# Optimization experiments

Measured on AMD Instinct MI355X. Metric: run time of the kernel, lower is better.

## Reference

```python
import jax, jax.numpy as jnp
import numpy as np

B, S, E = 4, 2048, 1024
H, D = 16, 64  # num_heads, attention_head_dim


def setup_inputs() -> dict:
    key = jax.random.key(0)
    ks = jax.random.split(key, 9)
    scale_e = 1.0 / np.sqrt(E)
    scale_hd = 1.0 / np.sqrt(H * D)
    x = jax.random.normal(ks[0], (B, S, E), dtype=jnp.float32)
    # per-head projection weights, stacked: [H, E, D]
    Wq = jax.random.uniform(ks[1], (H, E, D), minval=-scale_e, maxval=scale_e, dtype=jnp.float32)
    Wk = jax.random.uniform(ks[2], (H, E, D), minval=-scale_e, maxval=scale_e, dtype=jnp.float32)
    Wv = jax.random.uniform(ks[3], (H, E, D), minval=-scale_e, maxval=scale_e, dtype=jnp.float32)
    bq = jax.random.uniform(ks[4], (H, D), minval=-scale_e, maxval=scale_e, dtype=jnp.float32)
    bk = jax.random.uniform(ks[5], (H, D), minval=-scale_e, maxval=scale_e, dtype=jnp.float32)
    bv = jax.random.uniform(ks[6], (H, D), minval=-scale_e, maxval=scale_e, dtype=jnp.float32)
    Wo = jax.random.uniform(ks[7], (H * D, E), minval=-scale_hd, maxval=scale_hd, dtype=jnp.float32)
    bo = jax.random.uniform(ks[8], (E,), minval=-scale_hd, maxval=scale_hd, dtype=jnp.float32)
    return {"x": x, "Wq": Wq, "Wk": Wk, "Wv": Wv, "bq": bq, "bk": bk, "bv": bv, "Wo": Wo, "bo": bo}


def reference(x, Wq, Wk, Wv, bq, bk, bv, Wo, bo):
    # Per-head QKV projections, vectorized over heads: [B,H,S,D]
    Q = jnp.einsum('bse,hed->bhsd', x, Wq) + bq[None, :, None, :]
    K = jnp.einsum('bse,hed->bhsd', x, Wk) + bk[None, :, None, :]
    V = jnp.einsum('bse,hed->bhsd', x, Wv) + bv[None, :, None, :]
    scale = 1.0 / jnp.sqrt(jnp.asarray(D, dtype=Q.dtype))
    scores = jnp.einsum('bhsd,bhtd->bhst', Q, K) * scale  # [B,H,S,S]
    attn = jax.nn.softmax(scores, axis=-1)
    Z = jnp.einsum('bhst,bhtd->bhsd', attn, V)            # [B,H,S,D]
    # concat heads on feature dim -> [B,S,H*D], then output projection
    Zc = jnp.transpose(Z, (0, 2, 1, 3)).reshape(B, S, H * D)
    return Zc @ Wo + bo
```

## Files before the change

kernel.cpp:

```cpp
#include <hip/hip_runtime.h>


typedef __attribute__((ext_vector_type(4)))  float   f32x4;
typedef __attribute__((ext_vector_type(16))) float   f32x16;
typedef __attribute__((ext_vector_type(8)))  __bf16  bf16x8;
typedef __attribute__((ext_vector_type(4)))  __bf16  bf16x4;
typedef __attribute__((ext_vector_type(4)))  unsigned int u32x4;
typedef unsigned int u32;

#if __has_builtin(__builtin_amdgcn_exp2f)
#define EXP2F(x) __builtin_amdgcn_exp2f(x)
#else
#define EXP2F(x) exp2f(x)
#endif

__device__ __forceinline__ f32x4 fzero4() {
    f32x4 z = {0.f, 0.f, 0.f, 0.f};
    return z;
}
__device__ __forceinline__ f32x16 fzero16() {
    f32x16 z;
#pragma unroll
    for (int i = 0; i < 16; i++) z[i] = 0.f;
    return z;
}

__device__ __forceinline__ u32 cvtpk_bf16(float lo, float hi_) {
    u32 r;
    asm("v_cvt_pk_bf16_f32 %0, %1, %2" : "=v"(r) : "v"(lo), "v"(hi_));
    return r;
}

__device__ __forceinline__ void gload_lds16(const void* g, void* l) {
    __builtin_amdgcn_global_load_lds(
        (const __attribute__((address_space(1))) u32*)g,
        (__attribute__((address_space(3))) u32*)l, 16, 0, 0);
}

__global__ __launch_bounds__(256) void cvt_f32_bf16_4(
    const float* __restrict__ s, __bf16* __restrict__ d, long n) {
    long i = ((long)blockIdx.x * 256 + threadIdx.x) * 4;
    if (i >= n) return;
    float4 v = *(const float4*)(s + i);
    bf16x4 o = { (__bf16)v.x, (__bf16)v.y, (__bf16)v.z, (__bf16)v.w };
    *(bf16x4*)(d + i) = o;
}

__global__ __launch_bounds__(256) void pack_w_t(
    const float* __restrict__ src, __bf16* __restrict__ dst, int R, int C) {
    __shared__ float t[32][33];
    const int z = blockIdx.z;
    src += (size_t)z * R * C;
    dst += (size_t)z * R * C;
    const int r0 = blockIdx.x * 32, c0 = blockIdx.y * 32;
    const int x = threadIdx.x, y = threadIdx.y;
#pragma unroll
    for (int i = 0; i < 4; i++)
        t[y + i * 8][x] = src[(size_t)(r0 + y + i * 8) * C + c0 + x];
    __syncthreads();
#pragma unroll
    for (int i = 0; i < 4; i++)
        dst[(size_t)(c0 + y + i * 8) * R + r0 + x] = (__bf16)t[x][y + i * 8];
}

__global__ __launch_bounds__(256) void pack_bias(
    const float* __restrict__ bq, const float* __restrict__ bk,
    const float* __restrict__ bv, float* __restrict__ bqkv) {
    int n = blockIdx.x * 256 + threadIdx.x;
    if (n >= 3072) return;
    int t = n >> 10, r = n & 1023;
    const float* s = (t == 0) ? bq : (t == 1) ? bk : bv;
    bqkv[n] = s[r];
}

#define GEMM_STAGE(BUF, KOFF)                                                  \
  {                                                                            \
    gload_lds16(A + arow0 * K + (KOFF) + kcol,                                 \
                (char*)As + (BUF) * 16384 + wid * 1024);                       \
    gload_lds16(A + arow1 * K + (KOFF) + kcol,                                 \
                (char*)As + (BUF) * 16384 + 8192 + wid * 1024);                \
    gload_lds16(Bt + brow * K + (KOFF) + kcol,                                 \
                (char*)Bs + (BUF) * 8192 + wid * 1024);                        \
  }

#define GEMM_COMPUTE(BUF)                                                      \
  {                                                                            \
    bf16x8 a[4], b[4];                                                         \
    _Pragma("unroll")                                                          \
    for (int mi = 0; mi < 4; mi++)                                             \
      a[mi] = *(const bf16x8*)&As[(BUF) * 8192 +                               \
                                  (mr * 64 + mi * 16 + l15) * 32 + l4 * 8];    \
    _Pragma("unroll")                                                          \
    for (int ni = 0; ni < 4; ni++)                                             \
      b[ni] = *(const bf16x8*)&Bs[(BUF) * 4096 +                               \
                                  (nc * 64 + ni * 16 + l15) * 32 + l4 * 8];    \
    _Pragma("unroll")                                                          \
    for (int mi = 0; mi < 4; mi++)                                             \
      _Pragma("unroll")                                                        \
      for (int ni = 0; ni < 4; ni++)                                           \
        acc[mi][ni] = __builtin_amdgcn_mfma_f32_16x16x32_bf16(                 \
            a[mi], b[ni], acc[mi][ni], 0, 0, 0);                               \
  }

#define GEMM_PREAMBLE                                                          \
    const int tid  = threadIdx.x;                                              \
    const int lane = tid & 63, wid = tid >> 6;                                 \
    const int mr = wid >> 1, nc = wid & 1;                                     \
    const int l15 = lane & 15, l4 = lane >> 4;                                 \
    const int bn = blockIdx.x, bm = blockIdx.y;                                \
    const long arow0 = (long)bm * 256 + (tid >> 2);                            \
    const long arow1 = arow0 + 128;                                            \
    const long brow  = (long)bn * 128 + (tid >> 2);                            \
    const int  kcol  = (tid & 3) * 8;                                          \
    f32x4 acc[4][4];                                                           \
    _Pragma("unroll")                                                          \
    for (int i = 0; i < 4; i++)                                                \
      _Pragma("unroll")                                                        \
      for (int j = 0; j < 4; j++) acc[i][j] = fzero4();                        \
    GEMM_STAGE(0, 0)                                                           \
    __syncthreads();                                                           \
    int cur = 0;                                                               \
    for (int k0 = 0; k0 < K; k0 += 32, cur ^= 1) {                             \
        if (k0 + 32 < K) GEMM_STAGE(cur ^ 1, k0 + 32)                          \
        GEMM_COMPUTE(cur)                                                      \
        __syncthreads();                                                       \
    }

template <bool F32OUT>
__global__ __launch_bounds__(512) void gemm_bt(
    const __bf16* __restrict__ A, const __bf16* __restrict__ Bt,
    const float* __restrict__ bias, void* __restrict__ Cout,
    int M, int N, int K, int ldc) {
    __shared__ __bf16 As[2 * 256 * 32];
    __shared__ __bf16 Bs[2 * 128 * 32];
    GEMM_PREAMBLE

#pragma unroll
    for (int mi = 0; mi < 4; mi++)
#pragma unroll
        for (int ni = 0; ni < 4; ni++) {
            const int row = bm * 256 + mr * 64 + mi * 16 + l4 * 4;
            const int col = bn * 128 + nc * 64 + ni * 16 + l15;
            const float bv = bias ? bias[col] : 0.f;
#pragma unroll
            for (int r = 0; r < 4; r++) {
                float v = acc[mi][ni][r] + bv;
                if (F32OUT)
                    ((float*)Cout)[(long)(row + r) * ldc + col] = v;
                else
                    ((__bf16*)Cout)[(long)(row + r) * ldc + col] = (__bf16)v;
            }
        }
}

__global__ __launch_bounds__(512) void gemm_qkv(
    const __bf16* __restrict__ A, const __bf16* __restrict__ Bt,
    const float* __restrict__ bias, __bf16* __restrict__ QKV,
    __bf16* __restrict__ VT, int K) {
    __shared__ __bf16 As[2 * 256 * 32];
    __shared__ __bf16 Bs[2 * 128 * 32];
    GEMM_PREAMBLE

    if (bn < 16) {
#pragma unroll
        for (int mi = 0; mi < 4; mi++)
#pragma unroll
            for (int ni = 0; ni < 4; ni++) {
                const int row = bm * 256 + mr * 64 + mi * 16 + l4 * 4;
                const int col = bn * 128 + nc * 64 + ni * 16 + l15;
                const float bv = bias[col];
#pragma unroll
                for (int r = 0; r < 4; r++)
                    QKV[(long)(row + r) * 3072 + col] =
                        (__bf16)(acc[mi][ni][r] + bv);
            }
    } else {
#pragma unroll
        for (int mi = 0; mi < 4; mi++)
#pragma unroll
            for (int ni = 0; ni < 4; ni++) {
                const int row = bm * 256 + mr * 64 + mi * 16 + l4 * 4;
                const int col = bn * 128 + nc * 64 + ni * 16 + l15;
                const float bv = bias[col];
                const int vcol = col - 2048;
                const int h = vcol >> 6, dcol = vcol & 63;
                const int bb = row >> 11, s = row & 2047;
                bf16x4 o;
#pragma unroll
                for (int r = 0; r < 4; r++)
                    o[r] = (__bf16)(acc[mi][ni][r] + bv);
                *(bf16x4*)&VT[((size_t)(bb * 16 + h) * 64 + dcol) * 2048 + s] = o;
            }
    }
}

#define ATTN_SM_PV(S0, S1, M_R, L_R, O0, O1)                                   \
  {                                                                            \
    float mm[16];                                                              \
    _Pragma("unroll")                                                          \
    for (int i = 0; i < 16; i++) mm[i] = fmaxf(S0[i], S1[i]);                  \
    _Pragma("unroll")                                                          \
    for (int st = 8; st >= 1; st >>= 1)                                        \
      _Pragma("unroll")                                                        \
      for (int i = 0; i < st; i++) mm[i] = fmaxf(mm[i], mm[i + st]);           \
    const float pm = fmaxf(mm[0], __shfl_xor(mm[0], 32));                      \
    if (!__all(pm - M_R <= 64.f)) {              \
      const float mnew = fmaxf(M_R, pm);                                       \
      const float alpha = EXP2F((M_R - mnew) * csc);                           \
      M_R = mnew;                                                              \
      L_R *= alpha;                                                            \
      _Pragma("unroll")                                                        \
      for (int i = 0; i < 16; i++) { O0[i] *= alpha; O1[i] *= alpha; }         \
    }                                                                          \
    const float mc = M_R * csc;                                                \
    float ss[16];                                                              \
    _Pragma("unroll")                                                          \
    for (int i = 0; i < 16; i++) {                                             \
      float p0 = EXP2F(S0[i] * csc - mc); S0[i] = p0;                          \
      float p1 = EXP2F(S1[i] * csc - mc); S1[i] = p1;                          \
      ss[i] = p0 + p1;                                                         \
    }                                                                          \
    _Pragma("unroll")                                                          \
    for (int st = 8; st >= 1; st >>= 1)                                        \
      _Pragma("unroll")                                                        \
      for (int i = 0; i < st; i++) ss[i] += ss[i + st];                        \
    L_R += ss[0] + __shfl_xor(ss[0], 32);                                      \
    __builtin_amdgcn_s_setprio(1);                                             \
    _Pragma("unroll")                                                          \
    for (int kkt = 0; kkt < 4; kkt++) {                                        \
      const int r0 = (kkt & 1) * 8;                                            \
      u32 w0, w1, w2, w3;                                                      \
      if (kkt < 2) {                                                           \
        w0 = cvtpk_bf16(S0[r0],     S0[r0 + 1]);                               \
        w1 = cvtpk_bf16(S0[r0 + 2], S0[r0 + 3]);                               \
        w2 = cvtpk_bf16(S0[r0 + 4], S0[r0 + 5]);                               \
        w3 = cvtpk_bf16(S0[r0 + 6], S0[r0 + 7]);                               \
      } else {                                                                 \
        w0 = cvtpk_bf16(S1[r0],     S1[r0 + 1]);                               \
        w1 = cvtpk_bf16(S1[r0 + 2], S1[r0 + 3]);                               \
        w2 = cvtpk_bf16(S1[r0 + 4], S1[r0 + 5]);                               \
        w3 = cvtpk_bf16(S1[r0 + 6], S1[r0 + 7]);                               \
      }                                                                        \
      asm("v_permlane32_swap_b32 %0, %1" : "+v"(w0), "+v"(w2));                \
      asm("v_permlane32_swap_b32 %0, %1" : "+v"(w1), "+v"(w3));                \
      u32x4 pw = {w0, w1, w2, w3};                                             \
      bf16x8 pf = __builtin_bit_cast(bf16x8, pw);                              \
      O0 = __builtin_amdgcn_mfma_f32_32x32x16_bf16(vf[kkt],     pf, O0, 0, 0, 0); \
      O1 = __builtin_amdgcn_mfma_f32_32x32x16_bf16(vf[4 + kkt], pf, O1, 0, 0, 0); \
    }                                                                          \
    __builtin_amdgcn_s_setprio(0);                                             \
  }

#define ATTN_EPI(O0, O1, L_R, ROWBASE)                                         \
  {                                                                            \
    const float inv = 1.0f / L_R;                                              \
    _Pragma("unroll")                                                          \
    for (int g = 0; g < 4; g++) {                                              \
      bf16x4 t4a, t4b;                                                         \
      _Pragma("unroll")                                                        \
      for (int j = 0; j < 4; j++) {                                            \
        t4a[j] = (__bf16)(O0[4 * g + j] * inv);                                \
        t4b[j] = (__bf16)(O1[4 * g + j] * inv);                                \
      }                                                                        \
      *(bf16x4*)&Tl[trow][g * 8 + hi * 4]      = t4a;                          \
      *(bf16x4*)&Tl[trow][32 + g * 8 + hi * 4] = t4b;                          \
    }                                                                          \
    asm volatile("s_waitcnt lgkmcnt(0)" ::: "memory");                         \
    __builtin_amdgcn_sched_barrier(0);                                         \
    _Pragma("unroll")                                                          \
    for (int i = 0; i < 4; i++) {                                              \
      bf16x8 z = *(const bf16x8*)&Tl[rr][ch + i * 8];                          \
      *(bf16x8*)&Z[((size_t)b * S + (ROWBASE) + rr) * 1024 + h * 64 +          \
                   ch + i * 8] = z;                                            \
    }                                                                          \
    asm volatile("s_waitcnt lgkmcnt(0)" ::: "memory");                         \
    __builtin_amdgcn_sched_barrier(0);                                         \
  }

__global__ __launch_bounds__(256, 2) void attn_fwd(
    const __bf16* __restrict__ QKV, const __bf16* __restrict__ VT,
    __bf16* __restrict__ Z) {
    const int S = 2048, LDQ = 3072;
    const int dd = blockIdx.x;
    const int blk = (dd & 7) * 64 + (dd >> 3);
    const int qt = blk & 7, bh = blk >> 3, b = bh >> 4, h = bh & 15;
    const int tid = threadIdx.x, wid = tid >> 6, lane = tid & 63;
    const int l31 = lane & 31, hi = lane >> 5;

    __shared__ __bf16 smem[16384];

    const __bf16* Qb = QKV + (size_t)b * S * LDQ + h * 64;
    const __bf16* Kb = Qb + 1024;
    const __bf16* Vb = VT + (size_t)bh * 64 * S;
    const int qrowA = qt * 256 + wid * 32;
    const int qrowB = qrowA + 128;

    bf16x8 qfA[4], qfB[4];
#pragma unroll
    for (int kk = 0; kk < 4; kk++) {
        qfA[kk] = *(const bf16x8*)(Qb + (size_t)(qrowA + l31) * LDQ + kk * 16 + hi * 8);
        qfB[kk] = *(const bf16x8*)(Qb + (size_t)(qrowB + l31) * LDQ + kk * 16 + hi * 8);
    }

    const int f0 = wid * 2, f1 = wid * 2 + 1;
    const int kr0 = (f0 >> 2) * 32 + l31, kc0 = (f0 & 3) * 16 + hi * 8;
    const int kr1 = (f1 >> 2) * 32 + l31, kc1 = (f1 & 3) * 16 + hi * 8;
    const int vr0 = kr0, vs0 = kc0;
    const int vr1 = kr1, vs1 = kc1;
    const int ldst = lane * 16;

    f32x16 oA0 = fzero16(), oA1 = fzero16();
    f32x16 oB0 = fzero16(), oB1 = fzero16();
    float m_rA = -1e30f, l_rA = 0.f, m_rB = -1e30f, l_rB = 0.f;
    const float csc = 0.18033688011f;

    gload_lds16(Kb + (size_t)kr0 * LDQ + kc0, (char*)smem + f0 * 1024 + ldst);
    gload_lds16(Kb + (size_t)kr1 * LDQ + kc1, (char*)smem + f1 * 1024 + ldst);
    gload_lds16(Vb + (size_t)vr0 * S + vs0,   (char*)smem + 16384 + f0 * 1024 + ldst);
    gload_lds16(Vb + (size_t)vr1 * S + vs1,   (char*)smem + 16384 + f1 * 1024 + ldst);
    asm volatile("s_waitcnt vmcnt(0)" ::: "memory");
    __syncthreads();

    int cur = 0;
    for (int t0 = 0; t0 < S; t0 += 64, cur ^= 1) {
        if (t0 + 64 < S) {
            char* kl = (char*)smem + (cur ^ 1) * 8192;
            char* vl = (char*)smem + 16384 + (cur ^ 1) * 8192;
            gload_lds16(Kb + (size_t)(t0 + 64 + kr0) * LDQ + kc0, kl + f0 * 1024 + ldst);
            gload_lds16(Kb + (size_t)(t0 + 64 + kr1) * LDQ + kc1, kl + f1 * 1024 + ldst);
            gload_lds16(Vb + (size_t)vr0 * S + t0 + 64 + vs0,     vl + f0 * 1024 + ldst);
            gload_lds16(Vb + (size_t)vr1 * S + t0 + 64 + vs1,     vl + f1 * 1024 + ldst);
        }
        const char* kbase = (const char*)smem + cur * 8192;
        const char* vbase = (const char*)smem + 16384 + cur * 8192;

        bf16x8 kf[8];
#pragma unroll
        for (int f = 0; f < 8; f++)
            kf[f] = *(const bf16x8*)(kbase + f * 1024 + ldst);
        f32x16 sA0 = fzero16(), sA1 = fzero16();
        f32x16 sB0 = fzero16(), sB1 = fzero16();
        __builtin_amdgcn_s_setprio(1);
#pragma unroll
        for (int kk = 0; kk < 4; kk++) {
            sA0 = __builtin_amdgcn_mfma_f32_32x32x16_bf16(kf[kk],     qfA[kk], sA0, 0, 0, 0);
            sA1 = __builtin_amdgcn_mfma_f32_32x32x16_bf16(kf[4 + kk], qfA[kk], sA1, 0, 0, 0);
        }
#pragma unroll
        for (int kk = 0; kk < 4; kk++) {
            sB0 = __builtin_amdgcn_mfma_f32_32x32x16_bf16(kf[kk],     qfB[kk], sB0, 0, 0, 0);
            sB1 = __builtin_amdgcn_mfma_f32_32x32x16_bf16(kf[4 + kk], qfB[kk], sB1, 0, 0, 0);
        }
        __builtin_amdgcn_s_setprio(0);

        bf16x8 vf[8];
#pragma unroll
        for (int f = 0; f < 8; f++)
            vf[f] = *(const bf16x8*)(vbase + f * 1024 + ldst);

        ATTN_SM_PV(sA0, sA1, m_rA, l_rA, oA0, oA1)
        ATTN_SM_PV(sB0, sB1, m_rB, l_rB, oB0, oB1)

        asm volatile("s_waitcnt vmcnt(0)" ::: "memory");
        __syncthreads();
    }

    __bf16 (*Tl)[72] = (__bf16 (*)[72])smem;
    const int trow = wid * 32 + l31;
    const int rr = wid * 32 + (lane >> 1);
    const int ch = (lane & 1) * 32;
    ATTN_EPI(oA0, oA1, l_rA, qt * 256)
    ATTN_EPI(oB0, oB1, l_rB, qt * 256 + 128)
}

extern "C" void kernel_launch(void* const* d_in, const int* in_sizes, int n_in,
                              void* d_out, int out_size, void* d_ws, size_t ws_size,
                              hipStream_t stream) {
    const float* x  = (const float*)d_in[0];
    const float* Wq = (const float*)d_in[1];
    const float* Wk = (const float*)d_in[2];
    const float* Wv = (const float*)d_in[3];
    const float* bq = (const float*)d_in[4];
    const float* bk = (const float*)d_in[5];
    const float* bv = (const float*)d_in[6];
    const float* Wo = (const float*)d_in[7];
    const float* bo = (const float*)d_in[8];
    float* out = (float*)d_out;

    char* p = (char*)d_ws;
    __bf16* xb   = (__bf16*)p; p += 8192L * 1024 * 2;
    __bf16* Wqkv = (__bf16*)p; p += 3072L * 1024 * 2;
    float*  bqkv = (float*)p;  p += 3072L * 4;
    __bf16* QKV  = (__bf16*)p; p += 8192L * 3072 * 2;
    __bf16* VTb  = (__bf16*)p; p += 64L * 64 * 2048 * 2;
    __bf16* Zb   = (__bf16*)p; p += 8192L * 1024 * 2;
    __bf16* Wot  = (__bf16*)p; p += 1024L * 1024 * 2;

    cvt_f32_bf16_4<<<8192, 256, 0, stream>>>(x, xb, 8192L * 1024);
    pack_w_t<<<dim3(32, 2, 16), dim3(32, 8), 0, stream>>>(Wq, Wqkv,                1024, 64);
    pack_w_t<<<dim3(32, 2, 16), dim3(32, 8), 0, stream>>>(Wk, Wqkv + 1024L * 1024, 1024, 64);
    pack_w_t<<<dim3(32, 2, 16), dim3(32, 8), 0, stream>>>(Wv, Wqkv + 2048L * 1024, 1024, 64);
    pack_w_t<<<dim3(32, 32, 1), dim3(32, 8), 0, stream>>>(Wo, Wot, 1024, 1024);
    pack_bias<<<12, 256, 0, stream>>>(bq, bk, bv, bqkv);

    gemm_qkv<<<dim3(24, 32), 512, 0, stream>>>(xb, Wqkv, bqkv, QKV, VTb, 1024);
    attn_fwd<<<512, 256, 0, stream>>>(QKV, VTb, Zb);
    gemm_bt<true><<<dim3(8, 32), 512, 0, stream>>>(Zb, Wot, bo, out,
                                                   8192, 1024, 1024, 1024);
}
```

Baseline: 220.1 us.

## Fuse x fp32-to-bf16 conversion into QKV GEMM and remap block tiles per XCD

```diff
diff --git a/kernel.cpp b/kernel.cpp
--- a/kernel.cpp
+++ b/kernel.cpp
@@ -35,15 +35,6 @@
     __builtin_amdgcn_global_load_lds(
         (const __attribute__((address_space(1))) u32*)g,
         (__attribute__((address_space(3))) u32*)l, 16, 0, 0);
-}
-
-__global__ __launch_bounds__(256) void cvt_f32_bf16_4(
-    const float* __restrict__ s, __bf16* __restrict__ d, long n) {
-    long i = ((long)blockIdx.x * 256 + threadIdx.x) * 4;
-    if (i >= n) return;
-    float4 v = *(const float4*)(s + i);
-    bf16x4 o = { (__bf16)v.x, (__bf16)v.y, (__bf16)v.z, (__bf16)v.w };
-    *(bf16x4*)(d + i) = o;
 }
 
 __global__ __launch_bounds__(256) void pack_w_t(
@@ -72,6 +63,25 @@
     const float* s = (t == 0) ? bq : (t == 1) ? bk : bv;
     bqkv[n] = s[r];
 }
+
+#define GEMM_COMPUTE(BUF)                                                      \
+  {                                                                            \
+    bf16x8 a[4], b[4];                                                         \
+    _Pragma("unroll")                                                          \
+    for (int mi = 0; mi < 4; mi++)                                             \
+      a[mi] = *(const bf16x8*)&As[(BUF) * 8192 +                               \
+                                  (mr * 64 + mi * 16 + l15) * 32 + l4 * 8];    \
+    _Pragma("unroll")                                                          \
+    for (int ni = 0; ni < 4; ni++)                                             \
+      b[ni] = *(const bf16x8*)&Bs[(BUF) * 4096 +                               \
+                                  (nc * 64 + ni * 16 + l15) * 32 + l4 * 8];    \
+    _Pragma("unroll")                                                          \
+    for (int mi = 0; mi < 4; mi++)                                             \
+      _Pragma("unroll")                                                        \
+      for (int ni = 0; ni < 4; ni++)                                           \
+        acc[mi][ni] = __builtin_amdgcn_mfma_f32_16x16x32_bf16(                 \
+            a[mi], b[ni], acc[mi][ni], 0, 0, 0);                               \
+  }
 
 #define GEMM_STAGE(BUF, KOFF)                                                  \
   {                                                                            \
@@ -83,49 +93,6 @@
                 (char*)Bs + (BUF) * 8192 + wid * 1024);                        \
   }
 
-#define GEMM_COMPUTE(BUF)                                                      \
-  {                                                                            \
-    bf16x8 a[4], b[4];                                                         \
-    _Pragma("unroll")                                                          \
-    for (int mi = 0; mi < 4; mi++)                                             \
-      a[mi] = *(const bf16x8*)&As[(BUF) * 8192 +                               \
-                                  (mr * 64 + mi * 16 + l15) * 32 + l4 * 8];    \
-    _Pragma("unroll")                                                          \
-    for (int ni = 0; ni < 4; ni++)                                             \
-      b[ni] = *(const bf16x8*)&Bs[(BUF) * 4096 +                               \
-                                  (nc * 64 + ni * 16 + l15) * 32 + l4 * 8];    \
-    _Pragma("unroll")                                                          \
-    for (int mi = 0; mi < 4; mi++)                                             \
-      _Pragma("unroll")                                                        \
-      for (int ni = 0; ni < 4; ni++)                                           \
-        acc[mi][ni] = __builtin_amdgcn_mfma_f32_16x16x32_bf16(                 \
-            a[mi], b[ni], acc[mi][ni], 0, 0, 0);                               \
-  }
-
-#define GEMM_PREAMBLE                                                          \
-    const int tid  = threadIdx.x;                                              \
-    const int lane = tid & 63, wid = tid >> 6;                                 \
-    const int mr = wid >> 1, nc = wid & 1;                                     \
-    const int l15 = lane & 15, l4 = lane >> 4;                                 \
-    const int bn = blockIdx.x, bm = blockIdx.y;                                \
-    const long arow0 = (long)bm * 256 + (tid >> 2);                            \
-    const long arow1 = arow0 + 128;                                            \
-    const long brow  = (long)bn * 128 + (tid >> 2);                            \
-    const int  kcol  = (tid & 3) * 8;                                          \
-    f32x4 acc[4][4];                                                           \
-    _Pragma("unroll")                                                          \
-    for (int i = 0; i < 4; i++)                                                \
-      _Pragma("unroll")                                                        \
-      for (int j = 0; j < 4; j++) acc[i][j] = fzero4();                        \
-    GEMM_STAGE(0, 0)                                                           \
-    __syncthreads();                                                           \
-    int cur = 0;                                                               \
-    for (int k0 = 0; k0 < K; k0 += 32, cur ^= 1) {                             \
-        if (k0 + 32 < K) GEMM_STAGE(cur ^ 1, k0 + 32)                          \
-        GEMM_COMPUTE(cur)                                                      \
-        __syncthreads();                                                       \
-    }
-
 template <bool F32OUT>
 __global__ __launch_bounds__(512) void gemm_bt(
     const __bf16* __restrict__ A, const __bf16* __restrict__ Bt,
@@ -133,7 +100,31 @@
     int M, int N, int K, int ldc) {
     __shared__ __bf16 As[2 * 256 * 32];
     __shared__ __bf16 Bs[2 * 128 * 32];
-    GEMM_PREAMBLE
+    const int tid  = threadIdx.x;
+    const int lane = tid & 63, wid = tid >> 6;
+    const int mr = wid >> 1, nc = wid & 1;
+    const int l15 = lane & 15, l4 = lane >> 4;
+    const int dd = blockIdx.x;
+    const int idx = dd >> 3;
+    const int bm = (dd & 7) * 4 + (idx >> 3), bn = idx & 7;
+    const long arow0 = (long)bm * 256 + (tid >> 2);
+    const long arow1 = arow0 + 128;
+    const long brow  = (long)bn * 128 + (tid >> 2);
+    const int  kcol  = (tid & 3) * 8;
+    f32x4 acc[4][4];
+#pragma unroll
+    for (int i = 0; i < 4; i++)
+#pragma unroll
+        for (int j = 0; j < 4; j++) acc[i][j] = fzero4();
+
+    GEMM_STAGE(0, 0)
+    __syncthreads();
+    int cur = 0;
+    for (int k0 = 0; k0 < K; k0 += 32, cur ^= 1) {
+        if (k0 + 32 < K) GEMM_STAGE(cur ^ 1, k0 + 32)
+        GEMM_COMPUTE(cur)
+        __syncthreads();
+    }
 
 #pragma unroll
     for (int mi = 0; mi < 4; mi++)
@@ -153,13 +144,70 @@
         }
 }
 
+#define QKV_A_LOAD(KOFF)                                                       \
+    float4 a00 = *(const float4*)(Xr0 + (KOFF) + kcol);                        \
+    float4 a01 = *(const float4*)(Xr0 + (KOFF) + kcol + 4);                    \
+    float4 a10 = *(const float4*)(Xr1 + (KOFF) + kcol);                        \
+    float4 a11 = *(const float4*)(Xr1 + (KOFF) + kcol + 4);
+
+#define QKV_A_WRITE(BUF)                                                       \
+  {                                                                            \
+    bf16x8 w0 = {(__bf16)a00.x, (__bf16)a00.y, (__bf16)a00.z, (__bf16)a00.w,   \
+                 (__bf16)a01.x, (__bf16)a01.y, (__bf16)a01.z, (__bf16)a01.w};  \
+    bf16x8 w1 = {(__bf16)a10.x, (__bf16)a10.y, (__bf16)a10.z, (__bf16)a10.w,   \
+                 (__bf16)a11.x, (__bf16)a11.y, (__bf16)a11.z, (__bf16)a11.w};  \
+    *(bf16x8*)((char*)As + (BUF) * 16384 + tid * 16) = w0;                     \
+    *(bf16x8*)((char*)As + (BUF) * 16384 + 8192 + tid * 16) = w1;              \
+  }
+
+#define QKV_B_STAGE(BUF, KOFF)                                                 \
+    gload_lds16(Bt + brow * 1024 + (KOFF) + kcol,                              \
+                (char*)Bs + (BUF) * 8192 + wid * 1024);
+
 __global__ __launch_bounds__(512) void gemm_qkv(
-    const __bf16* __restrict__ A, const __bf16* __restrict__ Bt,
+    const float* __restrict__ X, const __bf16* __restrict__ Bt,
     const float* __restrict__ bias, __bf16* __restrict__ QKV,
-    __bf16* __restrict__ VT, int K) {
+    __bf16* __restrict__ VT) {
     __shared__ __bf16 As[2 * 256 * 32];
     __shared__ __bf16 Bs[2 * 128 * 32];
-    GEMM_PREAMBLE
+    const int tid  = threadIdx.x;
+    const int lane = tid & 63, wid = tid >> 6;
+    const int mr = wid >> 1, nc = wid & 1;
+    const int l15 = lane & 15, l4 = lane >> 4;
+    const int dd = blockIdx.x;
+    const int idx = dd >> 3;
+    const int bm = (dd & 7) * 4 + idx / 24, bn = idx % 24;
+    const long arow0 = (long)bm * 256 + (tid >> 2);
+    const long arow1 = arow0 + 128;
+    const long brow  = (long)bn * 128 + (tid >> 2);
+    const int  kcol  = (tid & 3) * 8;
+    const float* Xr0 = X + arow0 * 1024;
+    const float* Xr1 = X + arow1 * 1024;
+
+    f32x4 acc[4][4];
+#pragma unroll
+    for (int i = 0; i < 4; i++)
+#pragma unroll
+        for (int j = 0; j < 4; j++) acc[i][j] = fzero4();
+
+    {
+        QKV_A_LOAD(0)
+        QKV_B_STAGE(0, 0)
+        QKV_A_WRITE(0)
+    }
+    __syncthreads();
+    int cur = 0;
+    for (int k0 = 0; k0 < 1024; k0 += 32, cur ^= 1) {
+        if (k0 + 32 < 1024) {
+            QKV_A_LOAD(k0 + 32)
+            QKV_B_STAGE(cur ^ 1, k0 + 32)
+            GEMM_COMPUTE(cur)
+            QKV_A_WRITE(cur ^ 1)
+        } else {
+            GEMM_COMPUTE(cur)
+        }
+        __syncthreads();
+    }
 
     if (bn < 16) {
 #pragma unroll
@@ -388,7 +436,6 @@
     float* out = (float*)d_out;
 
     char* p = (char*)d_ws;
-    __bf16* xb   = (__bf16*)p; p += 8192L * 1024 * 2;
     __bf16* Wqkv = (__bf16*)p; p += 3072L * 1024 * 2;
     float*  bqkv = (float*)p;  p += 3072L * 4;
     __bf16* QKV  = (__bf16*)p; p += 8192L * 3072 * 2;
@@ -396,15 +443,14 @@
     __bf16* Zb   = (__bf16*)p; p += 8192L * 1024 * 2;
     __bf16* Wot  = (__bf16*)p; p += 1024L * 1024 * 2;
 
-    cvt_f32_bf16_4<<<8192, 256, 0, stream>>>(x, xb, 8192L * 1024);
     pack_w_t<<<dim3(32, 2, 16), dim3(32, 8), 0, stream>>>(Wq, Wqkv,                1024, 64);
     pack_w_t<<<dim3(32, 2, 16), dim3(32, 8), 0, stream>>>(Wk, Wqkv + 1024L * 1024, 1024, 64);
     pack_w_t<<<dim3(32, 2, 16), dim3(32, 8), 0, stream>>>(Wv, Wqkv + 2048L * 1024, 1024, 64);
     pack_w_t<<<dim3(32, 32, 1), dim3(32, 8), 0, stream>>>(Wo, Wot, 1024, 1024);
     pack_bias<<<12, 256, 0, stream>>>(bq, bk, bv, bqkv);
 
-    gemm_qkv<<<dim3(24, 32), 512, 0, stream>>>(xb, Wqkv, bqkv, QKV, VTb, 1024);
+    gemm_qkv<<<768, 512, 0, stream>>>(x, Wqkv, bqkv, QKV, VTb);
     attn_fwd<<<512, 256, 0, stream>>>(QKV, VTb, Zb);
-    gemm_bt<true><<<dim3(8, 32), 512, 0, stream>>>(Zb, Wot, bo, out,
-                                                   8192, 1024, 1024, 1024);
-}
+    gemm_bt<true><<<256, 512, 0, stream>>>(Zb, Wot, bo, out,
+                                           8192, 1024, 1024, 1024);
+}
```

New measurement: 268.6 us. 1.22x slower.
